# Optimization experiments

Hardware: AMD Instinct MI355X
Metric: run time of the kernel (lower is better)

The kernel has to match this reference:

```python
import jax, jax.numpy as jnp
import numpy as np

EMBED_DIM = 768
NUM_HEADS = 12
HEAD_DIM = EMBED_DIM // NUM_HEADS
B, S = 2, 2048


def setup_inputs() -> dict:
    key = jax.random.key(0)
    ks = jax.random.split(key, 6)
    glorot = jnp.sqrt(6.0 / (EMBED_DIM + EMBED_DIM)).astype(jnp.float32)
    x = jax.random.normal(ks[0], (B, S, EMBED_DIM), dtype=jnp.float32)
    mask = jnp.zeros((1, 1, S, S), dtype=jnp.float32)  # additive mask, 0 = no masking
    Wq = jax.random.uniform(ks[1], (EMBED_DIM, EMBED_DIM), jnp.float32, -glorot, glorot)
    Wk = jax.random.uniform(ks[2], (EMBED_DIM, EMBED_DIM), jnp.float32, -glorot, glorot)
    Wv = jax.random.uniform(ks[3], (EMBED_DIM, EMBED_DIM), jnp.float32, -glorot, glorot)
    Wo = jax.random.uniform(ks[4], (EMBED_DIM, EMBED_DIM), jnp.float32, -glorot, glorot)
    bo = jnp.zeros((EMBED_DIM,), dtype=jnp.float32)
    return {"x": x, "mask": mask, "Wq": Wq, "Wk": Wk, "Wv": Wv, "Wo": Wo, "bo": bo}


def reference(x, mask, Wq, Wk, Wv, Wo, bo):
    b, s, _ = x.shape
    # Q/K/V projections (no bias), split into heads: [b, h, s, d]
    def split_heads(t):
        return t.reshape(b, s, NUM_HEADS, HEAD_DIM).transpose(0, 2, 1, 3)
    q = split_heads(x @ Wq)
    k = split_heads(x @ Wk)
    v = split_heads(x @ Wv)
    scale = 1.0 / jnp.sqrt(jnp.float32(HEAD_DIM))
    logits = jnp.einsum('bhqd,bhkd->bhqk', q, k) * scale  # [b, h, s, s]
    logits = logits + mask * (-1e9)
    weights = jax.nn.softmax(logits, axis=-1)
    attn = jnp.einsum('bhqk,bhkd->bhqd', weights, v)
    concat = attn.transpose(0, 2, 1, 3).reshape(b, s, EMBED_DIM)
    return concat @ Wo + bo
```

## Files before the change

### kernel.cpp

```cpp
#include <hip/hip_runtime.h>


typedef __bf16 bf16_t;
typedef bf16_t bf16x8 __attribute__((ext_vector_type(8)));
typedef bf16_t bf16x4 __attribute__((ext_vector_type(4)));
typedef float f32x4 __attribute__((ext_vector_type(4)));
typedef _Float16 f16x4 __attribute__((ext_vector_type(4)));
typedef _Float16 f16x8 __attribute__((ext_vector_type(8)));
typedef __fp16 hf2 __attribute__((ext_vector_type(2)));

#define SC2 0.1803368801111137f
#define DEFER_THR 44.0f

__device__ __forceinline__ float bf2f(unsigned short u) {
  union { unsigned int i; float f; } x;
  x.i = ((unsigned int)u) << 16;
  return x.f;
}

__device__ __forceinline__ float fexp2(float x) {
  return __builtin_amdgcn_exp2f(x);
}

__device__ __forceinline__ void glds16(const bf16_t* g, bf16_t* l) {
  __builtin_amdgcn_global_load_lds(
      (const __attribute__((address_space(1))) void*)g,
      (__attribute__((address_space(3))) void*)l, 16, 0, 0);
}

__device__ __forceinline__ int detect_bf16_flag(const unsigned short* x) {
  const int lane = threadIdx.x & 63;
  const uint4* p = (const uint4*)x;
  uint4 a = p[lane * 2];
  uint4 b = p[lane * 2 + 1];
  unsigned int w[8] = {a.x, a.y, a.z, a.w, b.x, b.y, b.z, b.w};
  unsigned int big = 0;
#pragma unroll
  for (int i = 0; i < 8; i++) {
    unsigned int e0 = (w[i] >> 7) & 0xFF, e1 = (w[i] >> 23) & 0xFF;
    big |= (e0 > 0x88u) | (e1 > 0x88u);
  }
  unsigned long long bal = __ballot(big != 0u);
  return bal == 0ULL ? 1 : 0;
}

__global__ void k_prep(const void* __restrict__ x, const void* __restrict__ mask,
                       const void* __restrict__ Wq, const void* __restrict__ Wk,
                       const void* __restrict__ Wv, const void* __restrict__ Wo,
                       bf16_t* __restrict__ xb, bf16_t* __restrict__ wqkvT,
                       bf16_t* __restrict__ woT, int* __restrict__ mflags) {
  __shared__ float ts[32][33];
  __shared__ int snz;
  const int blk = blockIdx.x;
  const int f = detect_bf16_flag((const unsigned short*)x);

  if (blk < 1536) {
    if (f) return;
    int i = blk * 256 + threadIdx.x;
    const float* xf = (const float*)x + (size_t)i * 8;
    bf16x8 v;
#pragma unroll
    for (int j = 0; j < 8; j++) v[j] = (bf16_t)xf[j];
    *(bf16x8*)(xb + (size_t)i * 8) = v;
  } else if (blk < 3840) {
    const int t = blk - 1536;
    const int z = t / 576, r = t % 576, kt = r / 24, nt = r % 24;
    const void* wsrc = (z == 0) ? Wq : (z == 1) ? Wk : (z == 2) ? Wv : Wo;
    bf16_t* dst = (z < 3) ? (wqkvT + (size_t)z * 768 * 768) : woT;
    const int c = threadIdx.x & 31, r0 = threadIdx.x >> 5;
#pragma unroll
    for (int i = 0; i < 4; i++) {
      int kr = kt * 32 + r0 + i * 8;
      float v;
      if (f) v = bf2f(((const unsigned short*)wsrc)[(size_t)kr * 768 + nt * 32 + c]);
      else   v = ((const float*)wsrc)[(size_t)kr * 768 + nt * 32 + c];
      ts[r0 + i * 8][c] = v;
    }
    __syncthreads();
#pragma unroll
    for (int i = 0; i < 4; i++) {
      int nr = nt * 32 + r0 + i * 8;
      dst[(size_t)nr * 768 + kt * 32 + c] = (bf16_t)ts[c][r0 + i * 8];
    }
  } else {
    const int t = blk - 3840;
    const int qt = t >> 4, ktm = t & 15;
    if (threadIdx.x == 0) snz = 0;
    __syncthreads();
    unsigned int nz = 0;
    if (f) {
#pragma unroll
      for (int i = 0; i < 8; i++) {
        int uidx = i * 256 + threadIdx.x;
        int row = uidx >> 4, col = uidx & 15;
        const uint4* p = (const uint4*)((const char*)mask +
            ((size_t)(qt * 128 + row) * 2048 + ktm * 128) * 2 + col * 16);
        uint4 v = *p;
        nz |= ((v.x | v.y | v.z | v.w) & 0x7fff7fffu);
      }
    } else {
#pragma unroll
      for (int i = 0; i < 16; i++) {
        int uidx = i * 256 + threadIdx.x;
        int row = uidx >> 5, col = uidx & 31;
        const uint4* p = (const uint4*)((const char*)mask +
            ((size_t)(qt * 128 + row) * 2048 + ktm * 128) * 4 + col * 16);
        uint4 v = *p;
        nz |= ((v.x | v.y | v.z | v.w) & 0x7fffffffu);
      }
    }
    if (nz) snz = 1;
    __syncthreads();
    if (threadIdx.x == 0) mflags[qt * 16 + ktm] = snz;
  }
}

__global__ __launch_bounds__(256, 3) void k_gemmQKV(
    const bf16_t* __restrict__ xb, const bf16_t* __restrict__ Bm,
    bf16_t* __restrict__ Qd, char* __restrict__ Kd, char* __restrict__ Vt,
    const unsigned short* __restrict__ xdet) {
  __shared__ __align__(16) char smem[32768];
  _Float16* Tb = (_Float16*)smem;

  const int f = detect_bf16_flag(xdet);
  const bf16_t* A = f ? (const bf16_t*)xdet : xb;

  const int tid = threadIdx.x;
  const int n0 = blockIdx.x * 128, m0 = blockIdx.y * 128;
  const int r = tid >> 2, c8 = (tid & 3) << 3;
  const bf16_t* Ag = A + (size_t)(m0 + r) * 768 + c8;
  const bf16_t* Bg = Bm + (size_t)(n0 + r) * 768 + c8;
  const int wid = tid >> 6, lane = tid & 63;
  const int wm = (wid >> 1) << 6, wn = (wid & 1) << 6;
  const int lr = lane & 15, quad = lane >> 4, lk = quad << 3, g4 = quad << 2;

  f32x4 acc[4][4];
  const f32x4 z = {0.f, 0.f, 0.f, 0.f};
#pragma unroll
  for (int i = 0; i < 4; i++)
#pragma unroll
    for (int j = 0; j < 4; j++) acc[i][j] = z;

  {
    bf16_t* A0 = (bf16_t*)smem;
    bf16_t* B0 = (bf16_t*)(smem + 16384);
    glds16(Ag, A0 + wid * 512);
    glds16(Ag + (size_t)64 * 768, A0 + 2048 + wid * 512);
    glds16(Bg, B0 + wid * 512);
    glds16(Bg + (size_t)64 * 768, B0 + 2048 + wid * 512);
  }
  __syncthreads();

  for (int s = 0; s < 24; s++) {
    if (s < 23) {
      const int k0 = (s + 1) * 32;
      bf16_t* An = (bf16_t*)(smem + ((s + 1) & 1) * 8192);
      bf16_t* Bn = (bf16_t*)(smem + 16384 + ((s + 1) & 1) * 8192);
      glds16(Ag + k0, An + wid * 512);
      glds16(Ag + (size_t)64 * 768 + k0, An + 2048 + wid * 512);
      glds16(Bg + k0, Bn + wid * 512);
      glds16(Bg + (size_t)64 * 768 + k0, Bn + 2048 + wid * 512);
    }
    const bf16_t* As = (const bf16_t*)(smem + (s & 1) * 8192);
    const bf16_t* Bs = (const bf16_t*)(smem + 16384 + (s & 1) * 8192);
    bf16x8 af[4], bf_[4];
#pragma unroll
    for (int t = 0; t < 4; t++) af[t]  = *(const bf16x8*)&As[(wm + t * 16 + lr) * 32 + lk];
#pragma unroll
    for (int t = 0; t < 4; t++) bf_[t] = *(const bf16x8*)&Bs[(wn + t * 16 + lr) * 32 + lk];
#pragma unroll
    for (int i = 0; i < 4; i++)
#pragma unroll
      for (int j = 0; j < 4; j++)
        acc[i][j] = __builtin_amdgcn_mfma_f32_16x16x32_bf16(af[i], bf_[j], acc[i][j], 0, 0, 0);
    __syncthreads();
  }

  if (n0 < 768) {
    const int bb = m0 >> 11;
#pragma unroll
    for (int i = 0; i < 4; i++)
#pragma unroll
      for (int j = 0; j < 4; j++) {
        const int rc = n0 + wn + j * 16 + lr;
        const int hh = rc >> 6, dd = rc & 63;
        const size_t base = (((size_t)bb * 12 + hh) * 2048) * 64 + dd;
#pragma unroll
        for (int reg = 0; reg < 4; reg++) {
          const int s = (m0 & 2047) + wm + i * 16 + g4 + reg;
          Qd[base + (size_t)s * 64] = (bf16_t)acc[i][j][reg];
        }
      }
  } else if (n0 < 1536) {
    const int nb = n0 - 768;
    const int bb = m0 >> 11;
    const int g = ((m0 & 2047) + wm) >> 6;
#pragma unroll
    for (int i = 0; i < 4; i++) {
#pragma unroll
      for (int j = 0; j < 4; j++) {
        const int rc = nb + wn + j * 16 + lr;
        const int hh = rc >> 6, dd = rc & 63;
        const size_t tbase = ((size_t)((bb * 12 + hh) * 32 + g)) << 13;
        const int doff = ((dd >> 5) << 10) + (((dd >> 3) & 3) << 8) + ((dd & 7) << 1);
#pragma unroll
        for (int reg = 0; reg < 4; reg++) {
          const int sig = ((i >> 1) << 5) + ((quad & 1) << 4) +
                          (((((i & 1) << 1) | (quad >> 1))) << 2) + reg;
          *(bf16_t*)(Kd + tbase + ((sig >> 4) << 11) + ((sig & 15) << 4) + doff) =
              (bf16_t)acc[i][j][reg];
        }
      }
    }
  } else {
    const int bb = m0 >> 11;
#pragma unroll
    for (int half = 0; half < 2; half++) {
      if ((wid & 1) == half) {
#pragma unroll
        for (int j = 0; j < 4; j++) {
          const int d_l = j * 16 + lr;
#pragma unroll
          for (int i = 0; i < 4; i++)
#pragma unroll
            for (int reg = 0; reg < 4; reg++)
              Tb[d_l * 136 + wm + i * 16 + g4 + reg] = (_Float16)acc[i][j][reg];
        }
      }
      __syncthreads();
      const int row = tid >> 2, cc = (tid & 3) * 32;
      const int vcol = (n0 - 1536) + half * 64 + row;
      const int hh = vcol >> 6;
      const int g = ((m0 & 2047) + cc) >> 6;
      const int koff2 = (cc & 63) * 2;
      char* vb = Vt + (((size_t)((bb * 12 + hh) * 32 + g)) << 13) + (row << 7);
#pragma unroll
      for (int u = 0; u < 4; u++)
        *(uint4*)(vb + ((koff2 + u * 16) ^ ((row & 7) << 4))) =
            *(const uint4*)&Tb[row * 136 + cc + u * 8];
      __syncthreads();
    }
  }
}

__global__ __launch_bounds__(256, 3) void k_flash(
    const bf16_t* __restrict__ Qd, const char* __restrict__ Kd,
    const char* __restrict__ Vt, const void* __restrict__ mask,
    const int* __restrict__ mflags, const unsigned short* __restrict__ xdet,
    bf16_t* __restrict__ attn) {
  __shared__ __align__(16) char sm[32768];

  const int tid = threadIdx.x, wid = tid >> 6, lane = tid & 63;
  const int lr = lane & 15, quad = lane >> 4, lk = quad << 3, g4 = quad << 2;

  const int lin = blockIdx.x;
  const int gx = lin & 7, ww = lin >> 3;
  const int hb = gx * 3 + (ww >> 5);
  const int h = hb % 12, bb = hb / 12;
  const int qt = ww & 31;

  const size_t bh = (size_t)bb * 12 + h;
  const char* Kg = Kd + (bh << 18);
  const char* Vg = Vt + (bh << 18);

  const char* kgl = Kg + wid * 2048 + lane * 16;
  const char* vgl = Vg + wid * 2048 + lane * 16;

#define STAGE_K(t, p)                                                       \
  {                                                                         \
    const char* g_ = kgl + ((size_t)(t) << 13);                             \
    bf16_t* l_ = (bf16_t*)(sm + ((p) << 13) + wid * 2048);                  \
    glds16((const bf16_t*)g_, l_);                                          \
    glds16((const bf16_t*)(g_ + 1024), l_ + 512);                           \
  }
#define STAGE_V(t, p)                                                       \
  {                                                                         \
    const char* g_ = vgl + ((size_t)(t) << 13);                             \
    bf16_t* l_ = (bf16_t*)(sm + 16384 + ((p) << 13) + wid * 2048);          \
    glds16((const bf16_t*)g_, l_);                                          \
    glds16((const bf16_t*)(g_ + 1024), l_ + 512);                           \
  }

  STAGE_K(0, 0);
  STAGE_V(0, 0);
  STAGE_K(1, 1);

  const bf16_t* Qh = Qd + bh * 2048 * 64;
  const int q0 = qt * 64 + wid * 16;
  const int mbf = detect_bf16_flag(xdet);
  const int* mfrow = mflags + (qt >> 1) * 16;
  int mbits = 0;
#pragma unroll
  for (int t = 0; t < 16; t++) mbits |= (mfrow[t] != 0) << t;

  const bf16x8 qf0 = *(const bf16x8*)&Qh[(size_t)(q0 + lr) * 64 + lk];
  const bf16x8 qf1 = *(const bf16x8*)&Qh[(size_t)(q0 + lr) * 64 + 32 + lk];

  f16x8 ones8;
#pragma unroll
  for (int j = 0; j < 8; j++) ones8[j] = (_Float16)1.f;

  const int vxo0 = (quad * 16) ^ ((lr & 7) << 4);
  const int vxo1 = (64 + quad * 16) ^ ((lr & 7) << 4);

  const f32x4 z = {0.f, 0.f, 0.f, 0.f};
  f32x4 ot[4];
#pragma unroll
  for (int dt = 0; dt < 4; dt++) ot[dt] = z;
  float mrow = -1e30f, lrow = 0.f;

  __syncthreads();

  f32x4 svA[4], svB[4];
  {
#pragma unroll
    for (int ct = 0; ct < 4; ct++) svA[ct] = z;
#pragma unroll
    for (int ct = 0; ct < 4; ct++) {
      bf16x8 kf0 = *(const bf16x8*)(sm + ct * 2048 + lane * 16);
      bf16x8 kf1 = *(const bf16x8*)(sm + ct * 2048 + 1024 + lane * 16);
      svA[ct] = __builtin_amdgcn_mfma_f32_16x16x32_bf16(kf0, qf0, svA[ct], 0, 0, 0);
      svA[ct] = __builtin_amdgcn_mfma_f32_16x16x32_bf16(kf1, qf1, svA[ct], 0, 0, 0);
    }
  }
  __syncthreads();

#define FLASH_BODY(S, SVC, SVN)                                              \
  {                                                                          \
    const int s_ = (S);                                                      \
    if (s_ + 2 < 32) STAGE_K(s_ + 2, (s_) & 1);                              \
    if (s_ + 1 < 32) STAGE_V(s_ + 1, (s_ + 1) & 1);                          \
    if (s_ + 1 < 32) {                                                       \
      const char* Kn = sm + (((s_ + 1) & 1) << 13);                          \
      SVN[0] = z; SVN[1] = z; SVN[2] = z; SVN[3] = z;                        \
      __builtin_amdgcn_s_setprio(1);                                         \
      _Pragma("unroll")                                                      \
      for (int ct = 0; ct < 4; ct++) {                                       \
        bf16x8 kf0 = *(const bf16x8*)(Kn + ct * 2048 + lane * 16);           \
        bf16x8 kf1 = *(const bf16x8*)(Kn + ct * 2048 + 1024 + lane * 16);    \
        SVN[ct] = __builtin_amdgcn_mfma_f32_16x16x32_bf16(kf0, qf0, SVN[ct], 0, 0, 0); \
        SVN[ct] = __builtin_amdgcn_mfma_f32_16x16x32_bf16(kf1, qf1, SVN[ct], 0, 0, 0); \
      }                                                                      \
      __builtin_amdgcn_s_setprio(0);                                         \
    }                                                                        \
    if ((mbits >> (s_ >> 1)) & 1) {                                          \
      _Pragma("unroll")                                                      \
      for (int ct = 0; ct < 4; ct++) {                                       \
        _Pragma("unroll")                                                    \
        for (int reg = 0; reg < 4; reg++) {                                  \
          const int kk = ((ct >> 1) << 5) + (quad << 3) + ((ct & 1) << 2) + reg; \
          size_t mi = (size_t)(q0 + lr) * 2048 + s_ * 64 + kk;               \
          float mv = mbf ? bf2f(((const unsigned short*)mask)[mi])           \
                         : ((const float*)mask)[mi];                         \
          SVC[ct][reg] -= 8e9f * mv;                                         \
        }                                                                    \
      }                                                                      \
    }                                                                        \
    float t_ = fmaxf(                                                        \
        fmaxf(fmaxf(fmaxf(SVC[0][0], SVC[0][1]), fmaxf(SVC[0][2], SVC[0][3])), \
              fmaxf(fmaxf(SVC[1][0], SVC[1][1]), fmaxf(SVC[1][2], SVC[1][3]))), \
        fmaxf(fmaxf(fmaxf(SVC[2][0], SVC[2][1]), fmaxf(SVC[2][2], SVC[2][3])), \
              fmaxf(fmaxf(SVC[3][0], SVC[3][1]), fmaxf(SVC[3][2], SVC[3][3])))); \
    t_ = fmaxf(t_, __shfl_xor(t_, 16));                                      \
    t_ = fmaxf(t_, __shfl_xor(t_, 32));                                      \
    if (__ballot(t_ > mrow + DEFER_THR)) {                                   \
      const float mnew = fmaxf(mrow, t_);                                    \
      const float alpha = fexp2((mrow - mnew) * SC2);                        \
      _Pragma("unroll")                                                      \
      for (int dt = 0; dt < 4; dt++) {                                       \
        _Pragma("unroll")                                                    \
        for (int reg = 0; reg < 4; reg++) ot[dt][reg] *= alpha;              \
      }                                                                      \
      lrow *= alpha;                                                         \
      mrow = mnew;                                                           \
    }                                                                        \
    const float mS = mrow * SC2;                                             \
    f16x8 pb8[2];                                                            \
    _Pragma("unroll")                                                        \
    for (int c2 = 0; c2 < 2; c2++) {                                         \
      union { hf2 hh[4]; f16x8 v; } u;                                       \
      _Pragma("unroll")                                                      \
      for (int hh2 = 0; hh2 < 2; hh2++) {                                    \
        const int ct = c2 * 2 + hh2;                                         \
        float p0 = fexp2(fmaf(SVC[ct][0], SC2, -mS));                        \
        float p1 = fexp2(fmaf(SVC[ct][1], SC2, -mS));                        \
        float p2 = fexp2(fmaf(SVC[ct][2], SC2, -mS));                        \
        float p3 = fexp2(fmaf(SVC[ct][3], SC2, -mS));                        \
        u.hh[hh2 * 2 + 0] = __builtin_amdgcn_cvt_pkrtz(p0, p1);              \
        u.hh[hh2 * 2 + 1] = __builtin_amdgcn_cvt_pkrtz(p2, p3);              \
      }                                                                      \
      pb8[c2] = u.v;                                                         \
    }                                                                        \
    const char* Vc = sm + 16384 + ((s_ & 1) << 13);                          \
    f32x4 asum = z;                                                          \
    __builtin_amdgcn_s_setprio(1);                                           \
    _Pragma("unroll")                                                        \
    for (int c2 = 0; c2 < 2; c2++) {                                         \
      const int vxo = c2 ? vxo1 : vxo0;                                      \
      asum = __builtin_amdgcn_mfma_f32_16x16x32_f16(ones8, pb8[c2], asum, 0, 0, 0); \
      _Pragma("unroll")                                                      \
      for (int dt = 0; dt < 4; dt++) {                                       \
        f16x8 va = *(const f16x8*)(Vc + (dt * 16 + lr) * 128 + vxo);         \
        ot[dt] = __builtin_amdgcn_mfma_f32_16x16x32_f16(va, pb8[c2], ot[dt], 0, 0, 0); \
      }                                                                      \
    }                                                                        \
    __builtin_amdgcn_s_setprio(0);                                           \
    lrow += asum[0];                                                         \
    if (s_ < 31) __syncthreads();                                            \
  }

  for (int s2 = 0; s2 < 32; s2 += 2) {
    FLASH_BODY(s2, svA, svB);
    FLASH_BODY(s2 + 1, svB, svA);
  }
#undef FLASH_BODY
#undef STAGE_K
#undef STAGE_V

  const float inv = 1.0f / lrow;
  bf16_t* arow = attn + ((size_t)bb * 2048 + q0 + lr) * 768 + h * 64 + g4;
#pragma unroll
  for (int dt = 0; dt < 4; dt++) {
    bf16x4 v;
#pragma unroll
    for (int reg = 0; reg < 4; reg++) v[reg] = (bf16_t)(ot[dt][reg] * inv);
    *(bf16x4*)(arow + dt * 16) = v;
  }
}

__global__ __launch_bounds__(256, 3) void k_gemm2(
    const bf16_t* __restrict__ A, const bf16_t* __restrict__ Bm,
    const void* __restrict__ bo, const unsigned short* __restrict__ xdet,
    float* __restrict__ outF, unsigned short* __restrict__ outH) {
  __shared__ __align__(16) char smem[32768];

  const int tid = threadIdx.x, wid = tid >> 6, lane = tid & 63;
  const int n0 = blockIdx.x * 64, m0 = blockIdx.y * 64;
  const int wm = (wid >> 1) << 5, wn = (wid & 1) << 5;
  const int lr = lane & 15, lk = (lane >> 4) << 3, g4 = (lane >> 4) << 2;
  const bf16_t* Ag = A + (size_t)(m0 + (tid >> 2)) * 768 + ((tid & 3) << 3);
  const bf16_t* Bg = Bm + (size_t)(n0 + (tid >> 2)) * 768 + ((tid & 3) << 3);

  f32x4 acc[2][2];
  const f32x4 z = {0.f, 0.f, 0.f, 0.f};
#pragma unroll
  for (int i = 0; i < 2; i++)
#pragma unroll
    for (int j = 0; j < 2; j++) acc[i][j] = z;

  {
    bf16_t* A0 = (bf16_t*)smem;
    bf16_t* B0 = (bf16_t*)(smem + 16384);
    glds16(Ag, A0 + wid * 512);
    glds16(Ag + 32, A0 + 2048 + wid * 512);
    glds16(Bg, B0 + wid * 512);
    glds16(Bg + 32, B0 + 2048 + wid * 512);
  }
  __syncthreads();

  for (int s = 0; s < 12; s++) {
    if (s < 11) {
      const int k0 = (s + 1) * 64;
      bf16_t* An = (bf16_t*)(smem + ((s + 1) & 1) * 8192);
      bf16_t* Bn = (bf16_t*)(smem + 16384 + ((s + 1) & 1) * 8192);
      glds16(Ag + k0, An + wid * 512);
      glds16(Ag + k0 + 32, An + 2048 + wid * 512);
      glds16(Bg + k0, Bn + wid * 512);
      glds16(Bg + k0 + 32, Bn + 2048 + wid * 512);
    }
#pragma unroll
    for (int kc = 0; kc < 2; kc++) {
      const bf16_t* As = (const bf16_t*)(smem + (s & 1) * 8192) + kc * 2048;
      const bf16_t* Bs = (const bf16_t*)(smem + 16384 + (s & 1) * 8192) + kc * 2048;
      bf16x8 af[2], bf_[2];
#pragma unroll
      for (int i = 0; i < 2; i++) af[i]  = *(const bf16x8*)&As[(wm + i * 16 + lr) * 32 + lk];
#pragma unroll
      for (int j = 0; j < 2; j++) bf_[j] = *(const bf16x8*)&Bs[(wn + j * 16 + lr) * 32 + lk];
#pragma unroll
      for (int i = 0; i < 2; i++)
#pragma unroll
        for (int j = 0; j < 2; j++)
          acc[i][j] = __builtin_amdgcn_mfma_f32_16x16x32_bf16(af[i], bf_[j], acc[i][j], 0, 0, 0);
    }
    __syncthreads();
  }

  const int obf = detect_bf16_flag(xdet);
#pragma unroll
  for (int i = 0; i < 2; i++)
#pragma unroll
    for (int j = 0; j < 2; j++) {
      const int nn = n0 + wn + j * 16 + lr;
      const float bv = obf ? bf2f(((const unsigned short*)bo)[nn])
                           : ((const float*)bo)[nn];
#pragma unroll
      for (int reg = 0; reg < 4; reg++) {
        const int m = m0 + wm + i * 16 + g4 + reg;
        const float v = acc[i][j][reg] + bv;
        if (obf) outH[(size_t)m * 768 + nn] = __builtin_bit_cast(unsigned short, (bf16_t)v);
        else     outF[(size_t)m * 768 + nn] = v;
      }
    }
}

extern "C" void kernel_launch(void* const* d_in, const int* in_sizes, int n_in,
                              void* d_out, int out_size, void* d_ws, size_t ws_size,
                              hipStream_t stream) {
  (void)in_sizes; (void)n_in; (void)out_size; (void)ws_size;
  const void* x    = d_in[0];
  const void* mask = d_in[1];
  const void* Wq   = d_in[2];
  const void* Wk   = d_in[3];
  const void* Wv   = d_in[4];
  const void* Wo   = d_in[5];
  const void* bo   = d_in[6];

  char* w = (char*)d_ws;
  size_t off = 0;
  auto take = [&](size_t b) -> void* {
    void* p = w + off;
    off = (off + b + 255) & ~(size_t)255;
    return p;
  };
  int*      mflags = (int*)take(256 * 4);
  bf16_t*   wqkvT  = (bf16_t*)take((size_t)2304 * 768 * 2);
  bf16_t*   woT    = (bf16_t*)take((size_t)768 * 768 * 2);
  bf16_t*   xb     = (bf16_t*)take((size_t)4096 * 768 * 2);
  bf16_t*   Qd     = (bf16_t*)take((size_t)3145728 * 2);
  char*     Kd     = (char*)take((size_t)3145728 * 2);
  char*     Vt     = (char*)take((size_t)3145728 * 2);
  bf16_t*   attn   = xb;

  k_prep<<<4096, 256, 0, stream>>>(x, mask, Wq, Wk, Wv, Wo, xb, wqkvT, woT, mflags);
  k_gemmQKV<<<dim3(18, 32), 256, 0, stream>>>(xb, wqkvT, Qd, Kd, Vt,
                                              (const unsigned short*)x);
  k_flash<<<768, 256, 0, stream>>>(Qd, Kd, Vt, mask, mflags,
                                   (const unsigned short*)x, attn);
  k_gemm2<<<dim3(12, 64), 256, 0, stream>>>(attn, woT, bo, (const unsigned short*)x,
                                            (float*)d_out, (unsigned short*)d_out);
}
```

Measured before the change: 172.9 us.

## Split flash attention over two KV halves and merge partials in a new kernel

The flash kernel now splits each query tile's key range into two halves, which doubles the grid from 768 to 1536 blocks and raises the launch-bounds occupancy hint to 5. Each block writes unnormalized fp32 partial outputs plus its row max and sum, and a new merge kernel combines the two halves with a log-sum-exp rescale and writes bf16 attention. The aim is better CU fill on the many-CU GPU. The cost is an extra launch, a round trip of fp32 partials through global memory, and possible register spills under the tighter occupancy bound.

```diff
diff --git a/kernel.cpp b/kernel.cpp
--- a/kernel.cpp
+++ b/kernel.cpp
@@ -243,11 +243,11 @@
   }
 }
 
-__global__ __launch_bounds__(256, 3) void k_flash(
+__global__ __launch_bounds__(256, 5) void k_flash(
     const bf16_t* __restrict__ Qd, const char* __restrict__ Kd,
     const char* __restrict__ Vt, const void* __restrict__ mask,
     const int* __restrict__ mflags, const unsigned short* __restrict__ xdet,
-    bf16_t* __restrict__ attn) {
+    float* __restrict__ Opart, float* __restrict__ ml) {
   __shared__ __align__(16) char sm[32768];
 
   const int tid = threadIdx.x, wid = tid >> 6, lane = tid & 63;
@@ -255,13 +255,14 @@
 
   const int lin = blockIdx.x;
   const int gx = lin & 7, ww = lin >> 3;
-  const int hb = gx * 3 + (ww >> 5);
+  const int hb = gx * 3 + (ww >> 6);
   const int h = hb % 12, bb = hb / 12;
-  const int qt = ww & 31;
+  const int sub = ww & 63;
+  const int qt = sub >> 1, half = sub & 1;
 
   const size_t bh = (size_t)bb * 12 + h;
-  const char* Kg = Kd + (bh << 18);
-  const char* Vg = Vt + (bh << 18);
+  const char* Kg = Kd + (bh << 18) + ((size_t)half << 17);
+  const char* Vg = Vt + (bh << 18) + ((size_t)half << 17);
 
   const char* kgl = Kg + wid * 2048 + lane * 16;
   const char* vgl = Vg + wid * 2048 + lane * 16;
@@ -328,9 +329,9 @@
 #define FLASH_BODY(S, SVC, SVN)                                              \
   {                                                                          \
     const int s_ = (S);                                                      \
-    if (s_ + 2 < 32) STAGE_K(s_ + 2, (s_) & 1);                              \
-    if (s_ + 1 < 32) STAGE_V(s_ + 1, (s_ + 1) & 1);                          \
-    if (s_ + 1 < 32) {                                                       \
+    if (s_ + 2 < 16) STAGE_K(s_ + 2, (s_) & 1);                              \
+    if (s_ + 1 < 16) STAGE_V(s_ + 1, (s_ + 1) & 1);                          \
+    if (s_ + 1 < 16) {                                                       \
       const char* Kn = sm + (((s_ + 1) & 1) << 13);                          \
       SVN[0] = z; SVN[1] = z; SVN[2] = z; SVN[3] = z;                        \
       __builtin_amdgcn_s_setprio(1);                                         \
@@ -343,13 +344,14 @@
       }                                                                      \
       __builtin_amdgcn_s_setprio(0);                                         \
     }                                                                        \
-    if ((mbits >> (s_ >> 1)) & 1) {                                          \
+    const int gt_ = half * 16 + s_;                                          \
+    if ((mbits >> (gt_ >> 1)) & 1) {                                         \
       _Pragma("unroll")                                                      \
       for (int ct = 0; ct < 4; ct++) {                                       \
         _Pragma("unroll")                                                    \
         for (int reg = 0; reg < 4; reg++) {                                  \
           const int kk = ((ct >> 1) << 5) + (quad << 3) + ((ct & 1) << 2) + reg; \
-          size_t mi = (size_t)(q0 + lr) * 2048 + s_ * 64 + kk;               \
+          size_t mi = (size_t)(q0 + lr) * 2048 + gt_ * 64 + kk;              \
           float mv = mbf ? bf2f(((const unsigned short*)mask)[mi])           \
                          : ((const float*)mask)[mi];                         \
           SVC[ct][reg] -= 8e9f * mv;                                         \
@@ -406,10 +408,10 @@
     }                                                                        \
     __builtin_amdgcn_s_setprio(0);                                           \
     lrow += asum[0];                                                         \
-    if (s_ < 31) __syncthreads();                                            \
-  }
-
-  for (int s2 = 0; s2 < 32; s2 += 2) {
+    if (s_ < 15) __syncthreads();                                            \
+  }
+
+  for (int s2 = 0; s2 < 16; s2 += 2) {
     FLASH_BODY(s2, svA, svB);
     FLASH_BODY(s2 + 1, svB, svA);
   }
@@ -417,15 +419,49 @@
 #undef STAGE_K
 #undef STAGE_V
 
-  const float inv = 1.0f / lrow;
-  bf16_t* arow = attn + ((size_t)bb * 2048 + q0 + lr) * 768 + h * 64 + g4;
-#pragma unroll
-  for (int dt = 0; dt < 4; dt++) {
-    bf16x4 v;
-#pragma unroll
-    for (int reg = 0; reg < 4; reg++) v[reg] = (bf16_t)(ot[dt][reg] * inv);
-    *(bf16x4*)(arow + dt * 16) = v;
-  }
+  const size_t qrow = bh * 2048 + (size_t)(q0 + lr);
+  if (quad == 0) {
+    float2 v2; v2.x = mrow; v2.y = lrow;
+    *(float2*)(ml + qrow * 4 + half * 2) = v2;
+  }
+  float* orow = Opart + qrow * 128 + half * 64 + g4;
+#pragma unroll
+  for (int dt = 0; dt < 4; dt++)
+    *(f32x4*)(orow + dt * 16) = ot[dt];
+}
+
+__global__ __launch_bounds__(256) void k_merge(
+    const float* __restrict__ Opart, const float* __restrict__ ml,
+    bf16_t* __restrict__ attn) {
+  const int tid = threadIdx.x;
+  const int lin = blockIdx.x;
+  const int gx = lin & 7, ww = lin >> 3;
+  const int hb = gx * 3 + (ww >> 5);
+  const int seg = ww & 31;
+  const int h = hb % 12, bb = hb / 12;
+  const int r_local = tid >> 2, dchunk = (tid & 3) << 4;
+  const int qrow = seg * 64 + r_local;
+  const size_t grow = (size_t)hb * 2048 + qrow;
+
+  const float4 mlv = *(const float4*)(ml + grow * 4);
+  const float m = fmaxf(mlv.x, mlv.z);
+  const float w1 = fexp2((mlv.x - m) * SC2);
+  const float w2 = fexp2((mlv.z - m) * SC2);
+  const float inv = 1.0f / (w1 * mlv.y + w2 * mlv.w);
+
+  const float* o1 = Opart + grow * 128 + dchunk;
+  const float* o2 = o1 + 64;
+  bf16x8 out0, out1;
+#pragma unroll
+  for (int j = 0; j < 8; j++)
+    out0[j] = (bf16_t)((o1[j] * w1 + o2[j] * w2) * inv);
+#pragma unroll
+  for (int j = 0; j < 8; j++)
+    out1[j] = (bf16_t)((o1[8 + j] * w1 + o2[8 + j] * w2) * inv);
+
+  bf16_t* arow = attn + ((size_t)bb * 2048 + qrow) * 768 + h * 64 + dchunk;
+  *(bf16x8*)arow = out0;
+  *(bf16x8*)(arow + 8) = out1;
 }
 
 __global__ __launch_bounds__(256, 3) void k_gemm2(
@@ -530,13 +566,16 @@
   bf16_t*   Qd     = (bf16_t*)take((size_t)3145728 * 2);
   char*     Kd     = (char*)take((size_t)3145728 * 2);
   char*     Vt     = (char*)take((size_t)3145728 * 2);
+  float*    Opart  = (float*)take((size_t)49152 * 128 * 4);
+  float*    mlbuf  = (float*)take((size_t)49152 * 4 * 4);
   bf16_t*   attn   = xb;
 
   k_prep<<<4096, 256, 0, stream>>>(x, mask, Wq, Wk, Wv, Wo, xb, wqkvT, woT, mflags);
   k_gemmQKV<<<dim3(18, 32), 256, 0, stream>>>(xb, wqkvT, Qd, Kd, Vt,
                                               (const unsigned short*)x);
-  k_flash<<<768, 256, 0, stream>>>(Qd, Kd, Vt, mask, mflags,
-                                   (const unsigned short*)x, attn);
+  k_flash<<<1536, 256, 0, stream>>>(Qd, Kd, Vt, mask, mflags,
+                                    (const unsigned short*)x, Opart, mlbuf);
+  k_merge<<<768, 256, 0, stream>>>(Opart, mlbuf, attn);
   k_gemm2<<<dim3(12, 64), 256, 0, stream>>>(attn, woT, bo, (const unsigned short*)x,
                                             (float*)d_out, (unsigned short*)d_out);
 }
```

Result: slower. 274.3 us (+58.7%).

## Triple-buffer K/V tiles in LDS with partial vmcnt waits instead of full syncthreads

Applied to the files above, without the earlier changes.

Expands shared memory from 32KB to 48KB to hold three rotating K and three rotating V buffers. Prefetch distance grows by one tile, and each full __syncthreads is replaced by a partial vmcnt wait plus s_barrier, so loads for later tiles can stay in flight across iterations. The larger LDS footprint may reduce how many blocks fit per CU (launch bounds ask for 3). The loop also issues wrapped-around redundant loads on the last iterations.

```diff
diff --git a/kernel.cpp b/kernel.cpp
--- a/kernel.cpp
+++ b/kernel.cpp
@@ -248,7 +248,7 @@
     const char* __restrict__ Vt, const void* __restrict__ mask,
     const int* __restrict__ mflags, const unsigned short* __restrict__ xdet,
     bf16_t* __restrict__ attn) {
-  __shared__ __align__(16) char sm[32768];
+  __shared__ __align__(16) char sm[49152];
 
   const int tid = threadIdx.x, wid = tid >> 6, lane = tid & 63;
   const int lr = lane & 15, quad = lane >> 4, lk = quad << 3, g4 = quad << 2;
@@ -266,24 +266,29 @@
   const char* kgl = Kg + wid * 2048 + lane * 16;
   const char* vgl = Vg + wid * 2048 + lane * 16;
 
-#define STAGE_K(t, p)                                                       \
+#define STAGE_K(t, off)                                                     \
   {                                                                         \
     const char* g_ = kgl + ((size_t)(t) << 13);                             \
-    bf16_t* l_ = (bf16_t*)(sm + ((p) << 13) + wid * 2048);                  \
+    bf16_t* l_ = (bf16_t*)(sm + (off) + wid * 2048);                        \
     glds16((const bf16_t*)g_, l_);                                          \
     glds16((const bf16_t*)(g_ + 1024), l_ + 512);                           \
   }
-#define STAGE_V(t, p)                                                       \
+#define STAGE_V(t, off)                                                     \
   {                                                                         \
     const char* g_ = vgl + ((size_t)(t) << 13);                             \
-    bf16_t* l_ = (bf16_t*)(sm + 16384 + ((p) << 13) + wid * 2048);          \
+    bf16_t* l_ = (bf16_t*)(sm + (off) + wid * 2048);                        \
     glds16((const bf16_t*)g_, l_);                                          \
     glds16((const bf16_t*)(g_ + 1024), l_ + 512);                           \
   }
 
+  int ka = 0, kb = 8192, kc2 = 16384;
+  int va = 24576, vb2 = 32768, vc = 40960;
+
   STAGE_K(0, 0);
-  STAGE_V(0, 0);
-  STAGE_K(1, 1);
+  STAGE_V(0, 24576);
+  STAGE_K(1, 8192);
+  STAGE_V(1, 32768);
+  STAGE_K(2, 16384);
 
   const bf16_t* Qh = Qd + bh * 2048 * 64;
   const int q0 = qt * 64 + wid * 16;
@@ -309,7 +314,9 @@
   for (int dt = 0; dt < 4; dt++) ot[dt] = z;
   float mrow = -1e30f, lrow = 0.f;
 
-  __syncthreads();
+  asm volatile("s_waitcnt vmcnt(4)" ::: "memory");
+  __builtin_amdgcn_s_barrier();
+  __builtin_amdgcn_sched_barrier(0);
 
   f32x4 svA[4], svB[4];
   {
@@ -323,15 +330,16 @@
       svA[ct] = __builtin_amdgcn_mfma_f32_16x16x32_bf16(kf1, qf1, svA[ct], 0, 0, 0);
     }
   }
-  __syncthreads();
+  __builtin_amdgcn_s_barrier();
+  __builtin_amdgcn_sched_barrier(0);
 
 #define FLASH_BODY(S, SVC, SVN)                                              \
   {                                                                          \
     const int s_ = (S);                                                      \
-    if (s_ + 2 < 32) STAGE_K(s_ + 2, (s_) & 1);                              \
-    if (s_ + 1 < 32) STAGE_V(s_ + 1, (s_ + 1) & 1);                          \
+    STAGE_K((s_ + 3) & 31, ka);                                              \
+    STAGE_V((s_ + 2) & 31, vc);                                              \
     if (s_ + 1 < 32) {                                                       \
-      const char* Kn = sm + (((s_ + 1) & 1) << 13);                          \
+      const char* Kn = sm + kb;                                              \
       SVN[0] = z; SVN[1] = z; SVN[2] = z; SVN[3] = z;                        \
       __builtin_amdgcn_s_setprio(1);                                         \
       _Pragma("unroll")                                                      \
@@ -391,7 +399,7 @@
       }                                                                      \
       pb8[c2] = u.v;                                                         \
     }                                                                        \
-    const char* Vc = sm + 16384 + ((s_ & 1) << 13);                          \
+    const char* Vc = sm + va;                                                \
     f32x4 asum = z;                                                          \
     __builtin_amdgcn_s_setprio(1);                                           \
     _Pragma("unroll")                                                        \
@@ -400,13 +408,19 @@
       asum = __builtin_amdgcn_mfma_f32_16x16x32_f16(ones8, pb8[c2], asum, 0, 0, 0); \
       _Pragma("unroll")                                                      \
       for (int dt = 0; dt < 4; dt++) {                                       \
-        f16x8 va = *(const f16x8*)(Vc + (dt * 16 + lr) * 128 + vxo);         \
-        ot[dt] = __builtin_amdgcn_mfma_f32_16x16x32_f16(va, pb8[c2], ot[dt], 0, 0, 0); \
+        f16x8 va_ = *(const f16x8*)(Vc + (dt * 16 + lr) * 128 + vxo);        \
+        ot[dt] = __builtin_amdgcn_mfma_f32_16x16x32_f16(va_, pb8[c2], ot[dt], 0, 0, 0); \
       }                                                                      \
     }                                                                        \
     __builtin_amdgcn_s_setprio(0);                                           \
     lrow += asum[0];                                                         \
-    if (s_ < 31) __syncthreads();                                            \
+    if (s_ < 31) {                                                           \
+      asm volatile("s_waitcnt vmcnt(4)" ::: "memory");                       \
+      __builtin_amdgcn_s_barrier();                                          \
+      __builtin_amdgcn_sched_barrier(0);                                     \
+    }                                                                        \
+    { int t1 = ka; ka = kb; kb = kc2; kc2 = t1; }                            \
+    { int t2 = va; va = vb2; vb2 = vc; vc = t2; }                            \
   }
 
   for (int s2 = 0; s2 < 32; s2 += 2) {
```

Measured after the change: 172.8 us. About the same (-0.0%).

## Restructure flash attention to single-wave blocks loading K/V directly into registers

Applied to the files above, without the earlier changes.

The flash kernel now launches 64-thread single-wavefront blocks, each owning 32 query rows as two 16-row tiles. K and V fragments are loaded straight from global memory into registers, with the next K tile prefetched, so the shared-memory staging and per-step __syncthreads are gone. Each K/V fragment is reused across both query tiles to offset the lost cross-wave sharing through LDS. The trade-off is more global/L2 traffic per query row, since each wave fetches full K/V on its own, plus higher register pressure and fewer waves per CU (launch bounds 64,2).

```diff
diff --git a/kernel.cpp b/kernel.cpp
--- a/kernel.cpp
+++ b/kernel.cpp
@@ -243,58 +243,36 @@
   }
 }
 
-__global__ __launch_bounds__(256, 3) void k_flash(
+__global__ __launch_bounds__(64, 2) void k_flash(
     const bf16_t* __restrict__ Qd, const char* __restrict__ Kd,
     const char* __restrict__ Vt, const void* __restrict__ mask,
     const int* __restrict__ mflags, const unsigned short* __restrict__ xdet,
     bf16_t* __restrict__ attn) {
-  __shared__ __align__(16) char sm[32768];
-
-  const int tid = threadIdx.x, wid = tid >> 6, lane = tid & 63;
+  const int lane = threadIdx.x & 63;
   const int lr = lane & 15, quad = lane >> 4, lk = quad << 3, g4 = quad << 2;
 
   const int lin = blockIdx.x;
   const int gx = lin & 7, ww = lin >> 3;
-  const int hb = gx * 3 + (ww >> 5);
+  const int hb = gx * 3 + (ww >> 6);
   const int h = hb % 12, bb = hb / 12;
-  const int qt = ww & 31;
+  const int u = ww & 63;
+  const int q0 = u * 32;
 
   const size_t bh = (size_t)bb * 12 + h;
   const char* Kg = Kd + (bh << 18);
   const char* Vg = Vt + (bh << 18);
 
-  const char* kgl = Kg + wid * 2048 + lane * 16;
-  const char* vgl = Vg + wid * 2048 + lane * 16;
-
-#define STAGE_K(t, p)                                                       \
-  {                                                                         \
-    const char* g_ = kgl + ((size_t)(t) << 13);                             \
-    bf16_t* l_ = (bf16_t*)(sm + ((p) << 13) + wid * 2048);                  \
-    glds16((const bf16_t*)g_, l_);                                          \
-    glds16((const bf16_t*)(g_ + 1024), l_ + 512);                           \
-  }
-#define STAGE_V(t, p)                                                       \
-  {                                                                         \
-    const char* g_ = vgl + ((size_t)(t) << 13);                             \
-    bf16_t* l_ = (bf16_t*)(sm + 16384 + ((p) << 13) + wid * 2048);          \
-    glds16((const bf16_t*)g_, l_);                                          \
-    glds16((const bf16_t*)(g_ + 1024), l_ + 512);                           \
-  }
-
-  STAGE_K(0, 0);
-  STAGE_V(0, 0);
-  STAGE_K(1, 1);
-
   const bf16_t* Qh = Qd + bh * 2048 * 64;
-  const int q0 = qt * 64 + wid * 16;
   const int mbf = detect_bf16_flag(xdet);
-  const int* mfrow = mflags + (qt >> 1) * 16;
+  const int* mfrow = mflags + (u >> 2) * 16;
   int mbits = 0;
 #pragma unroll
   for (int t = 0; t < 16; t++) mbits |= (mfrow[t] != 0) << t;
 
-  const bf16x8 qf0 = *(const bf16x8*)&Qh[(size_t)(q0 + lr) * 64 + lk];
-  const bf16x8 qf1 = *(const bf16x8*)&Qh[(size_t)(q0 + lr) * 64 + 32 + lk];
+  const bf16x8 qfA0 = *(const bf16x8*)&Qh[(size_t)(q0 + lr) * 64 + lk];
+  const bf16x8 qfA1 = *(const bf16x8*)&Qh[(size_t)(q0 + lr) * 64 + 32 + lk];
+  const bf16x8 qfB0 = *(const bf16x8*)&Qh[(size_t)(q0 + 16 + lr) * 64 + lk];
+  const bf16x8 qfB1 = *(const bf16x8*)&Qh[(size_t)(q0 + 16 + lr) * 64 + 32 + lk];
 
   f16x8 ones8;
 #pragma unroll
@@ -304,127 +282,162 @@
   const int vxo1 = (64 + quad * 16) ^ ((lr & 7) << 4);
 
   const f32x4 z = {0.f, 0.f, 0.f, 0.f};
-  f32x4 ot[4];
-#pragma unroll
-  for (int dt = 0; dt < 4; dt++) ot[dt] = z;
-  float mrow = -1e30f, lrow = 0.f;
-
-  __syncthreads();
-
-  f32x4 svA[4], svB[4];
+  f32x4 otA[4], otB[4];
+#pragma unroll
+  for (int dt = 0; dt < 4; dt++) { otA[dt] = z; otB[dt] = z; }
+  float mA = -1e30f, lA = 0.f, mB = -1e30f, lB = 0.f;
+
+  bf16x8 kfP[8], kfQ[8];
   {
-#pragma unroll
-    for (int ct = 0; ct < 4; ct++) svA[ct] = z;
+    const char* K0 = Kg;
 #pragma unroll
     for (int ct = 0; ct < 4; ct++) {
-      bf16x8 kf0 = *(const bf16x8*)(sm + ct * 2048 + lane * 16);
-      bf16x8 kf1 = *(const bf16x8*)(sm + ct * 2048 + 1024 + lane * 16);
-      svA[ct] = __builtin_amdgcn_mfma_f32_16x16x32_bf16(kf0, qf0, svA[ct], 0, 0, 0);
-      svA[ct] = __builtin_amdgcn_mfma_f32_16x16x32_bf16(kf1, qf1, svA[ct], 0, 0, 0);
-    }
-  }
-  __syncthreads();
-
-#define FLASH_BODY(S, SVC, SVN)                                              \
+      kfP[ct * 2]     = *(const bf16x8*)(K0 + ct * 2048 + lane * 16);
+      kfP[ct * 2 + 1] = *(const bf16x8*)(K0 + ct * 2048 + 1024 + lane * 16);
+    }
+  }
+
+#define FLASH_BODY(S, KC, KN)                                                \
   {                                                                          \
     const int s_ = (S);                                                      \
-    if (s_ + 2 < 32) STAGE_K(s_ + 2, (s_) & 1);                              \
-    if (s_ + 1 < 32) STAGE_V(s_ + 1, (s_ + 1) & 1);                          \
+    const char* Vt_ = Vg + ((size_t)s_ << 13);                               \
+    f16x8 vf[8];                                                             \
+    _Pragma("unroll")                                                        \
+    for (int c2 = 0; c2 < 2; c2++) {                                         \
+      _Pragma("unroll")                                                      \
+      for (int dt = 0; dt < 4; dt++)                                         \
+        vf[c2 * 4 + dt] = *(const f16x8*)(Vt_ + (dt * 16 + lr) * 128 +       \
+                                          (c2 ? vxo1 : vxo0));               \
+    }                                                                        \
     if (s_ + 1 < 32) {                                                       \
-      const char* Kn = sm + (((s_ + 1) & 1) << 13);                          \
-      SVN[0] = z; SVN[1] = z; SVN[2] = z; SVN[3] = z;                        \
-      __builtin_amdgcn_s_setprio(1);                                         \
+      const char* Kn_ = Kg + ((size_t)(s_ + 1) << 13);                       \
       _Pragma("unroll")                                                      \
       for (int ct = 0; ct < 4; ct++) {                                       \
-        bf16x8 kf0 = *(const bf16x8*)(Kn + ct * 2048 + lane * 16);           \
-        bf16x8 kf1 = *(const bf16x8*)(Kn + ct * 2048 + 1024 + lane * 16);    \
-        SVN[ct] = __builtin_amdgcn_mfma_f32_16x16x32_bf16(kf0, qf0, SVN[ct], 0, 0, 0); \
-        SVN[ct] = __builtin_amdgcn_mfma_f32_16x16x32_bf16(kf1, qf1, SVN[ct], 0, 0, 0); \
+        KN[ct * 2]     = *(const bf16x8*)(Kn_ + ct * 2048 + lane * 16);      \
+        KN[ct * 2 + 1] = *(const bf16x8*)(Kn_ + ct * 2048 + 1024 + lane * 16); \
       }                                                                      \
-      __builtin_amdgcn_s_setprio(0);                                         \
-    }                                                                        \
+    }                                                                        \
+    f32x4 svA[4], svB[4];                                                    \
+    _Pragma("unroll")                                                        \
+    for (int ct = 0; ct < 4; ct++) { svA[ct] = z; svB[ct] = z; }             \
+    __builtin_amdgcn_s_setprio(1);                                           \
+    _Pragma("unroll")                                                        \
+    for (int ct = 0; ct < 4; ct++) {                                         \
+      svA[ct] = __builtin_amdgcn_mfma_f32_16x16x32_bf16(KC[ct * 2], qfA0, svA[ct], 0, 0, 0); \
+      svA[ct] = __builtin_amdgcn_mfma_f32_16x16x32_bf16(KC[ct * 2 + 1], qfA1, svA[ct], 0, 0, 0); \
+      svB[ct] = __builtin_amdgcn_mfma_f32_16x16x32_bf16(KC[ct * 2], qfB0, svB[ct], 0, 0, 0); \
+      svB[ct] = __builtin_amdgcn_mfma_f32_16x16x32_bf16(KC[ct * 2 + 1], qfB1, svB[ct], 0, 0, 0); \
+    }                                                                        \
+    __builtin_amdgcn_s_setprio(0);                                           \
     if ((mbits >> (s_ >> 1)) & 1) {                                          \
       _Pragma("unroll")                                                      \
       for (int ct = 0; ct < 4; ct++) {                                       \
         _Pragma("unroll")                                                    \
         for (int reg = 0; reg < 4; reg++) {                                  \
           const int kk = ((ct >> 1) << 5) + (quad << 3) + ((ct & 1) << 2) + reg; \
-          size_t mi = (size_t)(q0 + lr) * 2048 + s_ * 64 + kk;               \
-          float mv = mbf ? bf2f(((const unsigned short*)mask)[mi])           \
-                         : ((const float*)mask)[mi];                         \
-          SVC[ct][reg] -= 8e9f * mv;                                         \
+          size_t miA = (size_t)(q0 + lr) * 2048 + s_ * 64 + kk;              \
+          size_t miB = (size_t)(q0 + 16 + lr) * 2048 + s_ * 64 + kk;         \
+          float mvA = mbf ? bf2f(((const unsigned short*)mask)[miA])         \
+                          : ((const float*)mask)[miA];                       \
+          float mvB = mbf ? bf2f(((const unsigned short*)mask)[miB])         \
+                          : ((const float*)mask)[miB];                       \
+          svA[ct][reg] -= 8e9f * mvA;                                        \
+          svB[ct][reg] -= 8e9f * mvB;                                        \
         }                                                                    \
       }                                                                      \
     }                                                                        \
-    float t_ = fmaxf(                                                        \
-        fmaxf(fmaxf(fmaxf(SVC[0][0], SVC[0][1]), fmaxf(SVC[0][2], SVC[0][3])), \
-              fmaxf(fmaxf(SVC[1][0], SVC[1][1]), fmaxf(SVC[1][2], SVC[1][3]))), \
-        fmaxf(fmaxf(fmaxf(SVC[2][0], SVC[2][1]), fmaxf(SVC[2][2], SVC[2][3])), \
-              fmaxf(fmaxf(SVC[3][0], SVC[3][1]), fmaxf(SVC[3][2], SVC[3][3])))); \
-    t_ = fmaxf(t_, __shfl_xor(t_, 16));                                      \
-    t_ = fmaxf(t_, __shfl_xor(t_, 32));                                      \
-    if (__ballot(t_ > mrow + DEFER_THR)) {                                   \
-      const float mnew = fmaxf(mrow, t_);                                    \
-      const float alpha = fexp2((mrow - mnew) * SC2);                        \
+    float tA = fmaxf(                                                        \
+        fmaxf(fmaxf(fmaxf(svA[0][0], svA[0][1]), fmaxf(svA[0][2], svA[0][3])), \
+              fmaxf(fmaxf(svA[1][0], svA[1][1]), fmaxf(svA[1][2], svA[1][3]))), \
+        fmaxf(fmaxf(fmaxf(svA[2][0], svA[2][1]), fmaxf(svA[2][2], svA[2][3])), \
+              fmaxf(fmaxf(svA[3][0], svA[3][1]), fmaxf(svA[3][2], svA[3][3])))); \
+    float tB = fmaxf(                                                        \
+        fmaxf(fmaxf(fmaxf(svB[0][0], svB[0][1]), fmaxf(svB[0][2], svB[0][3])), \
+              fmaxf(fmaxf(svB[1][0], svB[1][1]), fmaxf(svB[1][2], svB[1][3]))), \
+        fmaxf(fmaxf(fmaxf(svB[2][0], svB[2][1]), fmaxf(svB[2][2], svB[2][3])), \
+              fmaxf(fmaxf(svB[3][0], svB[3][1]), fmaxf(svB[3][2], svB[3][3])))); \
+    tA = fmaxf(tA, __shfl_xor(tA, 16));                                      \
+    tA = fmaxf(tA, __shfl_xor(tA, 32));                                      \
+    tB = fmaxf(tB, __shfl_xor(tB, 16));                                      \
+    tB = fmaxf(tB, __shfl_xor(tB, 32));                                      \
+    if (__ballot(tA > mA + DEFER_THR)) {                                     \
+      const float mnew = fmaxf(mA, tA);                                      \
+      const float alpha = fexp2((mA - mnew) * SC2);                          \
       _Pragma("unroll")                                                      \
       for (int dt = 0; dt < 4; dt++) {                                       \
         _Pragma("unroll")                                                    \
-        for (int reg = 0; reg < 4; reg++) ot[dt][reg] *= alpha;              \
+        for (int reg = 0; reg < 4; reg++) otA[dt][reg] *= alpha;             \
       }                                                                      \
-      lrow *= alpha;                                                         \
-      mrow = mnew;                                                           \
-    }                                                                        \
-    const float mS = mrow * SC2;                                             \
-    f16x8 pb8[2];                                                            \
+      lA *= alpha; mA = mnew;                                                \
+    }                                                                        \
+    if (__ballot(tB > mB + DEFER_THR)) {                                     \
+      const float mnew = fmaxf(mB, tB);                                      \
+      const float alpha = fexp2((mB - mnew) * SC2);                          \
+      _Pragma("unroll")                                                      \
+      for (int dt = 0; dt < 4; dt++) {                                       \
+        _Pragma("unroll")                                                    \
+        for (int reg = 0; reg < 4; reg++) otB[dt][reg] *= alpha;             \
+      }                                                                      \
+      lB *= alpha; mB = mnew;                                                \
+    }                                                                        \
+    const float mSA = mA * SC2, mSB = mB * SC2;                              \
+    f16x8 pbA[2], pbB[2];                                                    \
     _Pragma("unroll")                                                        \
     for (int c2 = 0; c2 < 2; c2++) {                                         \
-      union { hf2 hh[4]; f16x8 v; } u;                                       \
+      union { hf2 hh[4]; f16x8 v; } uA, uB;                                  \
       _Pragma("unroll")                                                      \
       for (int hh2 = 0; hh2 < 2; hh2++) {                                    \
         const int ct = c2 * 2 + hh2;                                         \
-        float p0 = fexp2(fmaf(SVC[ct][0], SC2, -mS));                        \
-        float p1 = fexp2(fmaf(SVC[ct][1], SC2, -mS));                        \
-        float p2 = fexp2(fmaf(SVC[ct][2], SC2, -mS));                        \
-        float p3 = fexp2(fmaf(SVC[ct][3], SC2, -mS));                        \
-        u.hh[hh2 * 2 + 0] = __builtin_amdgcn_cvt_pkrtz(p0, p1);              \
-        u.hh[hh2 * 2 + 1] = __builtin_amdgcn_cvt_pkrtz(p2, p3);              \
+        float a0 = fexp2(fmaf(svA[ct][0], SC2, -mSA));                       \
+        float a1 = fexp2(fmaf(svA[ct][1], SC2, -mSA));                       \
+        float a2 = fexp2(fmaf(svA[ct][2], SC2, -mSA));                       \
+        float a3 = fexp2(fmaf(svA[ct][3], SC2, -mSA));                       \
+        float b0 = fexp2(fmaf(svB[ct][0], SC2, -mSB));                       \
+        float b1 = fexp2(fmaf(svB[ct][1], SC2, -mSB));                       \
+        float b2 = fexp2(fmaf(svB[ct][2], SC2, -mSB));                       \
+        float b3 = fexp2(fmaf(svB[ct][3], SC2, -mSB));                       \
+        uA.hh[hh2 * 2 + 0] = __builtin_amdgcn_cvt_pkrtz(a0, a1);             \
+        uA.hh[hh2 * 2 + 1] = __builtin_amdgcn_cvt_pkrtz(a2, a3);             \
+        uB.hh[hh2 * 2 + 0] = __builtin_amdgcn_cvt_pkrtz(b0, b1);             \
+        uB.hh[hh2 * 2 + 1] = __builtin_amdgcn_cvt_pkrtz(b2, b3);             \
       }                                                                      \
-      pb8[c2] = u.v;                                                         \
-    }                                                                        \
-    const char* Vc = sm + 16384 + ((s_ & 1) << 13);                          \
-    f32x4 asum = z;                                                          \
+      pbA[c2] = uA.v; pbB[c2] = uB.v;                                        \
+    }                                                                        \
+    f32x4 asumA = z, asumB = z;                                              \
     __builtin_amdgcn_s_setprio(1);                                           \
     _Pragma("unroll")                                                        \
     for (int c2 = 0; c2 < 2; c2++) {                                         \
-      const int vxo = c2 ? vxo1 : vxo0;                                      \
-      asum = __builtin_amdgcn_mfma_f32_16x16x32_f16(ones8, pb8[c2], asum, 0, 0, 0); \
+      asumA = __builtin_amdgcn_mfma_f32_16x16x32_f16(ones8, pbA[c2], asumA, 0, 0, 0); \
+      asumB = __builtin_amdgcn_mfma_f32_16x16x32_f16(ones8, pbB[c2], asumB, 0, 0, 0); \
       _Pragma("unroll")                                                      \
       for (int dt = 0; dt < 4; dt++) {                                       \
-        f16x8 va = *(const f16x8*)(Vc + (dt * 16 + lr) * 128 + vxo);         \
-        ot[dt] = __builtin_amdgcn_mfma_f32_16x16x32_f16(va, pb8[c2], ot[dt], 0, 0, 0); \
+        otA[dt] = __builtin_amdgcn_mfma_f32_16x16x32_f16(vf[c2 * 4 + dt], pbA[c2], otA[dt], 0, 0, 0); \
+        otB[dt] = __builtin_amdgcn_mfma_f32_16x16x32_f16(vf[c2 * 4 + dt], pbB[c2], otB[dt], 0, 0, 0); \
       }                                                                      \
     }                                                                        \
     __builtin_amdgcn_s_setprio(0);                                           \
-    lrow += asum[0];                                                         \
-    if (s_ < 31) __syncthreads();                                            \
+    lA += asumA[0]; lB += asumB[0];                                          \
   }
 
   for (int s2 = 0; s2 < 32; s2 += 2) {
-    FLASH_BODY(s2, svA, svB);
-    FLASH_BODY(s2 + 1, svB, svA);
+    FLASH_BODY(s2, kfP, kfQ);
+    FLASH_BODY(s2 + 1, kfQ, kfP);
   }
 #undef FLASH_BODY
-#undef STAGE_K
-#undef STAGE_V
-
-  const float inv = 1.0f / lrow;
-  bf16_t* arow = attn + ((size_t)bb * 2048 + q0 + lr) * 768 + h * 64 + g4;
+
+  const float invA = 1.0f / lA, invB = 1.0f / lB;
+  bf16_t* arowA = attn + ((size_t)bb * 2048 + q0 + lr) * 768 + h * 64 + g4;
+  bf16_t* arowB = attn + ((size_t)bb * 2048 + q0 + 16 + lr) * 768 + h * 64 + g4;
 #pragma unroll
   for (int dt = 0; dt < 4; dt++) {
-    bf16x4 v;
-#pragma unroll
-    for (int reg = 0; reg < 4; reg++) v[reg] = (bf16_t)(ot[dt][reg] * inv);
-    *(bf16x4*)(arow + dt * 16) = v;
+    bf16x4 vA, vB;
+#pragma unroll
+    for (int reg = 0; reg < 4; reg++) {
+      vA[reg] = (bf16_t)(otA[dt][reg] * invA);
+      vB[reg] = (bf16_t)(otB[dt][reg] * invB);
+    }
+    *(bf16x4*)(arowA + dt * 16) = vA;
+    *(bf16x4*)(arowB + dt * 16) = vB;
   }
 }
 
@@ -535,7 +548,7 @@
   k_prep<<<4096, 256, 0, stream>>>(x, mask, Wq, Wk, Wv, Wo, xb, wqkvT, woT, mflags);
   k_gemmQKV<<<dim3(18, 32), 256, 0, stream>>>(xb, wqkvT, Qd, Kd, Vt,
                                               (const unsigned short*)x);
-  k_flash<<<768, 256, 0, stream>>>(Qd, Kd, Vt, mask, mflags,
+  k_flash<<<1536, 64, 0, stream>>>(Qd, Kd, Vt, mask, mflags,
                                    (const unsigned short*)x, attn);
   k_gemm2<<<dim3(12, 64), 256, 0, stream>>>(attn, woT, bo, (const unsigned short*)x,
                                             (float*)d_out, (unsigned short*)d_out);
```

After: 175.5 us. Within noise of the previous version (+1.5%).
